# Kernel optimization log

Measured on AMD Instinct MI355X. Metric: run time of the kernel, lower is better.

The kernel has to match this reference:

```python
import jax, jax.numpy as jnp
import numpy as np

B, S, D, R, H = 4, 2048, 1024, 256, 8
NI, NP, NO, K = 8, 32, 8, 3
DH = R // H


def _householder_chain(x, vs):
    # x: [B,S,R], vs: [B,S,K,R]; apply K Householder reflections sequentially
    def step(carry, v):
        vn = v * jax.lax.rsqrt(jnp.sum(v * v, axis=-1, keepdims=True) + 1e-8)
        vTx = jnp.sum(carry * vn, axis=-1, keepdims=True)
        return carry - 2.0 * vn * vTx, None
    out, _ = jax.lax.scan(step, x, jnp.moveaxis(vs, 2, 0))
    return out


def _circuit_down(x, in_neurons, proc_neurons, input_weights, proc_idx):
    # soft mixture of input-neuron projections: d_model -> rank
    all_proj = jnp.einsum('bsd,ndr->bsnr', x, in_neurons)
    xr = jnp.einsum('bsnr,bsn->bsr', all_proj, input_weights)
    return _householder_chain(xr, proc_neurons[proc_idx])


def setup_inputs():
    key = jax.random.key(0)
    ks = jax.random.split(key, 14)
    n = lambda k, shape, sc: jax.random.normal(k, shape, jnp.float32) * sc
    inv_d, inv_r = 1.0 / np.sqrt(D), 1.0 / np.sqrt(R)
    return {
        'x': n(ks[0], (B, S, D), 1.0),
        'q_in': n(ks[1], (NI, D, R), inv_d),
        'q_proc': n(ks[2], (NP, R), inv_r),
        'k_in': n(ks[3], (NI, D, R), inv_d),
        'k_proc': n(ks[4], (NP, R), inv_r),
        'v_in': n(ks[5], (NI, D, R), inv_d),
        'v_proc': n(ks[6], (NP, R), inv_r),
        'o_proc': n(ks[7], (NP, R), inv_r),
        'o_out': n(ks[8], (NO, R, D), inv_r),
        'rd_in': n(ks[9], (NI, D), inv_d),
        'rd_proc': n(ks[10], (NP, D), inv_d),
        'ru_out': n(ks[11], (NO, R), inv_r),
        'ru_proc': n(ks[12], (NP, R), inv_r),
    }


def reference(x, q_in, q_proc, k_in, k_proc, v_in, v_proc, o_proc, o_out,
              rd_in, rd_proc, ru_out, ru_proc):
    # --- router (down): soft input weights + top-k process indices ---
    input_weights = jax.nn.softmax(x @ rd_in.T, axis=-1)          # [B,S,NI]
    _, pidx = jax.lax.top_k(x @ rd_proc.T, K)                     # [B,S,K]

    q = _circuit_down(x, q_in, q_proc, input_weights, pidx)      # [B,S,R]
    k = _circuit_down(x, k_in, k_proc, input_weights, pidx)
    v = _circuit_down(x, v_in, v_proc, input_weights, pidx)

    qh = q.reshape(B, S, H, DH)
    kh = k.reshape(B, S, H, DH)
    vh = v.reshape(B, S, H, DH)
    scores = jnp.einsum('bqhd,bkhd->bhqk', qh, kh) / np.sqrt(DH)
    attn = jax.nn.softmax(scores, axis=-1)
    o = jnp.einsum('bhqk,bkhd->bqhd', attn, vh).reshape(B, S, R)  # [B,S,R]

    # --- router (up): soft output weights + top-k process indices ---
    output_weights = jax.nn.softmax(o @ ru_out.T, axis=-1)        # [B,S,NO]
    _, pidx_u = jax.lax.top_k(o @ ru_proc.T, K)                   # [B,S,K]

    oh = _householder_chain(o, o_proc[pidx_u])                    # [B,S,R]
    out = jnp.einsum('bsr,bsn,nrd->bsd', oh, output_weights, o_out)
    return out
```

## Files before the change

kernel.cpp:

```cpp
#include <hip/hip_runtime.h>
#include <math.h>

#define NI 8
#define NP 32
#define TOPK 3

typedef _Float16 f16;
typedef f16 f16x8 __attribute__((ext_vector_type(8)));
typedef f16 f16x4 __attribute__((ext_vector_type(4)));
typedef float f32x4 __attribute__((ext_vector_type(4)));

__device__ __forceinline__ float wave_sum(float v) {
  #pragma unroll
  for (int off = 32; off; off >>= 1) v += __shfl_xor(v, off);
  return v;
}

__device__ __forceinline__ void gload16(const void* g, void* l) {
  __builtin_amdgcn_global_load_lds(
      (const __attribute__((address_space(1))) unsigned int*)g,
      (__attribute__((address_space(3))) unsigned int*)l, 16, 0, 0);
}

__device__ __forceinline__ void split4(float4 v, f16x4& h, f16x4& l) {
  h[0] = (f16)v.x; l[0] = (f16)(v.x - (float)h[0]);
  h[1] = (f16)v.y; l[1] = (f16)(v.y - (float)h[1]);
  h[2] = (f16)v.z; l[2] = (f16)(v.z - (float)h[2]);
  h[3] = (f16)v.w; l[3] = (f16)(v.w - (float)h[3]);
}

__device__ __forceinline__ unsigned int pack_f16x2(float x) {
  f16 h = (f16)x;
  f16 l = (f16)(x - (float)h);
  return (unsigned int)__builtin_bit_cast(unsigned short, h)
       | ((unsigned int)__builtin_bit_cast(unsigned short, l) << 16);
}

__device__ __forceinline__ void unpack8(const unsigned int* p, f16x8& hi, f16x8& lo) {
  uint4 w0 = *reinterpret_cast<const uint4*>(p);
  uint4 w1 = *reinterpret_cast<const uint4*>(p + 4);
  union { unsigned int u[4]; f16x8 v; } H, L;
  H.u[0] = (w0.x & 0xffffu) | (w0.y << 16);
  L.u[0] = (w0.x >> 16)     | (w0.y & 0xffff0000u);
  H.u[1] = (w0.z & 0xffffu) | (w0.w << 16);
  L.u[1] = (w0.z >> 16)     | (w0.w & 0xffff0000u);
  H.u[2] = (w1.x & 0xffffu) | (w1.y << 16);
  L.u[2] = (w1.x >> 16)     | (w1.y & 0xffff0000u);
  H.u[3] = (w1.z & 0xffffu) | (w1.w << 16);
  L.u[3] = (w1.z >> 16)     | (w1.w & 0xffff0000u);
  hi = H.v; lo = L.v;
}

template<int CHUNKS>
__global__ __launch_bounds__(256) void router_v2(
    const float* __restrict__ X,
    const float* __restrict__ Wsm,
    const float* __restrict__ Wtk,
    float* __restrict__ iw, int* __restrict__ pidx,
    f16* __restrict__ Xh, f16* __restrict__ Xl)
{
  const int Kin = CHUNKS * 256;
  const int tid = threadIdx.x, wave = tid >> 6, lane = tid & 63;
  __shared__ float sc[4][4][40];
  const size_t t0 = (size_t)blockIdx.x * 16 + wave * 4;

  float4 xv[4][CHUNKS];
  #pragma unroll
  for (int tt = 0; tt < 4; ++tt) {
    const float4* Xp = reinterpret_cast<const float4*>(X + (t0 + tt) * Kin);
    #pragma unroll
    for (int c = 0; c < CHUNKS; ++c) xv[tt][c] = Xp[c * 64 + lane];
  }
  if (Xh) {
    #pragma unroll
    for (int tt = 0; tt < 4; ++tt)
      #pragma unroll
      for (int c = 0; c < CHUNKS; ++c) {
        f16x4 h, l;
        split4(xv[tt][c], h, l);
        size_t off = (t0 + tt) * Kin + (c * 64 + lane) * 4;
        *reinterpret_cast<f16x4*>(Xh + off) = h;
        *reinterpret_cast<f16x4*>(Xl + off) = l;
      }
  }

  for (int w = 0; w < 40; ++w) {
    const float* Wr = (w < NI) ? (Wsm + (size_t)w * Kin) : (Wtk + (size_t)(w - NI) * Kin);
    const float4* Wp = reinterpret_cast<const float4*>(Wr);
    float p[4] = {};
    #pragma unroll
    for (int c = 0; c < CHUNKS; ++c) {
      float4 wv = Wp[c * 64 + lane];
      #pragma unroll
      for (int tt = 0; tt < 4; ++tt) {
        p[tt] = fmaf(xv[tt][c].x, wv.x, p[tt]);
        p[tt] = fmaf(xv[tt][c].y, wv.y, p[tt]);
        p[tt] = fmaf(xv[tt][c].z, wv.z, p[tt]);
        p[tt] = fmaf(xv[tt][c].w, wv.w, p[tt]);
      }
    }
    #pragma unroll
    for (int tt = 0; tt < 4; ++tt) {
      p[tt] = wave_sum(p[tt]);
      if (lane == 0) sc[wave][tt][w] = p[tt];
    }
  }

  for (int tt = 0; tt < 4; ++tt) {
    float s = (lane < NI) ? sc[wave][tt][lane] : -3.0e38f;
    float m = s;
    #pragma unroll
    for (int off = 4; off; off >>= 1) m = fmaxf(m, __shfl_xor(m, off));
    float e = expf(s - m);
    float sum = e;
    #pragma unroll
    for (int off = 4; off; off >>= 1) sum += __shfl_xor(sum, off);
    if (lane < NI) iw[(t0 + tt) * NI + lane] = e / sum;

    float v = (lane < NP) ? sc[wave][tt][NI + lane] : -3.0e38f;
    int idx = lane;
    #pragma unroll
    for (int j = 0; j < TOPK; ++j) {
      float bv = v; int bi = idx;
      #pragma unroll
      for (int off = 32; off; off >>= 1) {
        float ov = __shfl_xor(bv, off); int oi = __shfl_xor(bi, off);
        if (ov > bv || (ov == bv && oi < bi)) { bv = ov; bi = oi; }
      }
      if (lane == 0) pidx[(t0 + tt) * TOPK + j] = bi;
      if (idx == bi) v = -3.0e38f;
    }
  }
}

__global__ __launch_bounds__(256) void router_hh_up(
    const float* __restrict__ O,
    const float* __restrict__ Wsm,
    const float* __restrict__ Wtk,
    const float* __restrict__ Pm,
    float* __restrict__ owt, int* __restrict__ pidxu,
    f16* __restrict__ Oh, f16* __restrict__ Ol)
{
  const int tid = threadIdx.x, wave = tid >> 6, lane = tid & 63;
  __shared__ float sc[4][4][40];
  const size_t t0 = (size_t)blockIdx.x * 16 + wave * 4;

  float4 xv[4];
  #pragma unroll
  for (int tt = 0; tt < 4; ++tt)
    xv[tt] = *reinterpret_cast<const float4*>(O + (t0 + tt) * 256 + lane * 4);

  for (int w = 0; w < 40; ++w) {
    const float* Wr = (w < NI) ? (Wsm + (size_t)w * 256) : (Wtk + (size_t)(w - NI) * 256);
    float4 wv = *reinterpret_cast<const float4*>(Wr + lane * 4);
    float p[4];
    #pragma unroll
    for (int tt = 0; tt < 4; ++tt) {
      float q = 0.f;
      q = fmaf(xv[tt].x, wv.x, q); q = fmaf(xv[tt].y, wv.y, q);
      q = fmaf(xv[tt].z, wv.z, q); q = fmaf(xv[tt].w, wv.w, q);
      p[tt] = wave_sum(q);
    }
    #pragma unroll
    for (int tt = 0; tt < 4; ++tt)
      if (lane == 0) sc[wave][tt][w] = p[tt];
  }

  for (int tt = 0; tt < 4; ++tt) {
    float s = (lane < NI) ? sc[wave][tt][lane] : -3.0e38f;
    float m = s;
    #pragma unroll
    for (int off = 4; off; off >>= 1) m = fmaxf(m, __shfl_xor(m, off));
    float e = expf(s - m);
    float sum = e;
    #pragma unroll
    for (int off = 4; off; off >>= 1) sum += __shfl_xor(sum, off);
    if (lane < NI) owt[(t0 + tt) * NI + lane] = e / sum;

    float v = (lane < NP) ? sc[wave][tt][NI + lane] : -3.0e38f;
    int idx = lane;
    int pid[TOPK];
    #pragma unroll
    for (int j = 0; j < TOPK; ++j) {
      float bv = v; int bi = idx;
      #pragma unroll
      for (int off = 32; off; off >>= 1) {
        float ov = __shfl_xor(bv, off); int oi = __shfl_xor(bi, off);
        if (ov > bv || (ov == bv && oi < bi)) { bv = ov; bi = oi; }
      }
      pid[j] = bi;
      if (lane == 0) pidxu[(t0 + tt) * TOPK + j] = bi;
      if (idx == bi) v = -3.0e38f;
    }

    float4 x4 = xv[tt];
    #pragma unroll
    for (int j = 0; j < TOPK; ++j) {
      const float* vp = Pm + (size_t)pid[j] * 256;
      float4 v4 = *reinterpret_cast<const float4*>(vp + lane * 4);
      float ss = v4.x * v4.x + v4.y * v4.y + v4.z * v4.z + v4.w * v4.w;
      ss = wave_sum(ss);
      float inv = 1.0f / sqrtf(ss + 1e-8f);
      float4 vn = {v4.x * inv, v4.y * inv, v4.z * inv, v4.w * inv};
      float dt = vn.x * x4.x + vn.y * x4.y + vn.z * x4.z + vn.w * x4.w;
      dt = wave_sum(dt);
      float d2 = 2.0f * dt;
      x4.x = fmaf(-d2, vn.x, x4.x);
      x4.y = fmaf(-d2, vn.y, x4.y);
      x4.z = fmaf(-d2, vn.z, x4.z);
      x4.w = fmaf(-d2, vn.w, x4.w);
    }
    f16x4 h, l;
    split4(x4, h, l);
    *reinterpret_cast<f16x4*>(Oh + (t0 + tt) * 256 + lane * 4) = h;
    *reinterpret_cast<f16x4*>(Ol + (t0 + tt) * 256 + lane * 4) = l;
  }
}

__global__ __launch_bounds__(256) void pack_bt(
    const float* __restrict__ S, f16* __restrict__ Dh, f16* __restrict__ Dl,
    int C, int K)
{
  __shared__ float T[64][65];
  const int tid = threadIdx.x;
  const int kb = blockIdx.x * 64, cb = blockIdx.y * 64;
  const int tr = tid >> 4, tc = (tid & 15) * 4;
  #pragma unroll
  for (int i = 0; i < 4; ++i) {
    float4 v = *reinterpret_cast<const float4*>(&S[(size_t)(kb + tr + i * 16) * C + cb + tc]);
    T[tr + i * 16][tc + 0] = v.x; T[tr + i * 16][tc + 1] = v.y;
    T[tr + i * 16][tc + 2] = v.z; T[tr + i * 16][tc + 3] = v.w;
  }
  __syncthreads();
  #pragma unroll
  for (int i = 0; i < 4; ++i) {
    int c = tr + i * 16;
    f16x4 vh, vl;
    #pragma unroll
    for (int q = 0; q < 4; ++q) {
      float a = T[tc + q][c];
      f16 h = (f16)a;
      vh[q] = h;
      vl[q] = (f16)(a - (float)h);
    }
    *reinterpret_cast<f16x4*>(&Dh[(size_t)(cb + c) * K + kb + tc]) = vh;
    *reinterpret_cast<f16x4*>(&Dl[(size_t)(cb + c) * K + kb + tc]) = vl;
  }
}

#define TBM 128
#define TBK 32

template<int NFRAG>
__global__ __launch_bounds__(256, 3) void gemm_split2(
    const f16* __restrict__ Xh, const f16* __restrict__ Xl, int Kin,
    const float* __restrict__ W,
    const f16* __restrict__ Bth, const f16* __restrict__ Btl,
    float* __restrict__ C, int ldC, int Ktot)
{
  const int TBN = 32 * NFRAG;
  __shared__ f16x8 AhL[512];
  __shared__ f16x8 AlL[512];
  __shared__ f16x8 BhL[TBN * 4];
  __shared__ f16x8 BlL[TBN * 4];
  __shared__ float Ws[TBM][NI];

  const int tid = threadIdx.x;
  const int wave = tid >> 6, lane = tid & 63;
  const int wm = wave >> 1, wn = wave & 1;
  const int fr = lane & 15, ks = lane >> 4;
  const int row0 = blockIdx.x * TBM, c0 = blockIdx.y * TBN;

  for (int i = tid; i < TBM * NI; i += 256)
    Ws[i >> 3][i & 7] = W[(size_t)(row0 + (i >> 3)) * NI + (i & 7)];

  const int s1 = 256 + tid;
  const int ar0 = tid >> 2, kg0 = ((tid & 3) - (ar0 >> 1)) & 3;
  const int ar1 = s1 >> 2,  kg1 = ((s1 & 3) - (ar1 >> 1)) & 3;

  const f16* xh0 = Xh + (size_t)(row0 + ar0) * Kin + kg0 * 8;
  const f16* xh1 = Xh + (size_t)(row0 + ar1) * Kin + kg1 * 8;
  const f16* xl0 = Xl + (size_t)(row0 + ar0) * Kin + kg0 * 8;
  const f16* xl1 = Xl + (size_t)(row0 + ar1) * Kin + kg1 * 8;
  const f16* bh0 = Bth + (size_t)(c0 + ar0) * Ktot + kg0 * 8;
  const f16* bl0 = Btl + (size_t)(c0 + ar0) * Ktot + kg0 * 8;
  const int ar1b = (ar1 < TBN) ? ar1 : 0;
  const f16* bh1 = Bth + (size_t)(c0 + ar1b) * Ktot + kg1 * 8;
  const f16* bl1 = Btl + (size_t)(c0 + ar1b) * Ktot + kg1 * 8;
  const bool b2 = (NFRAG == 4) || (NFRAG == 3 && wave < 2);

  f16x8* AhW = &AhL[wave * 64];
  f16x8* AlW = &AlL[wave * 64];
  f16x8* BhW = &BhL[wave * 64];
  f16x8* BlW = &BlL[wave * 64];

  f32x4 acc[4][NFRAG] = {};
  f32x4 cac[4][NFRAG] = {};

  int n = 0, dk0 = 0;
  for (int kt = 0; kt < Ktot; kt += TBK) {
    __syncthreads();
    gload16(xh0 + dk0, AhW);
    gload16(xh1 + dk0, AhW + 256);
    gload16(xl0 + dk0, AlW);
    gload16(xl1 + dk0, AlW + 256);
    gload16(bh0 + kt, BhW);
    gload16(bl0 + kt, BlW);
    if (b2) {
      gload16(bh1 + kt, BhW + 256);
      gload16(bl1 + kt, BlW + 256);
    }
    __syncthreads();

    f16x8 ah[4], al[4], bh[NFRAG], bl[NFRAG];
    #pragma unroll
    for (int mf = 0; mf < 4; ++mf) {
      int ar = wm * 64 + mf * 16 + fr;
      int sl = ar * 4 + (((ar >> 1) + ks) & 3);
      ah[mf] = AhL[sl]; al[mf] = AlL[sl];
    }
    #pragma unroll
    for (int nf = 0; nf < NFRAG; ++nf) {
      int bc = wn * (16 * NFRAG) + nf * 16 + fr;
      int sl = bc * 4 + (((bc >> 1) + ks) & 3);
      bh[nf] = BhL[sl]; bl[nf] = BlL[sl];
    }
    #pragma unroll
    for (int mf = 0; mf < 4; ++mf)
      #pragma unroll
      for (int nf = 0; nf < NFRAG; ++nf) {
        acc[mf][nf] = __builtin_amdgcn_mfma_f32_16x16x32_f16(ah[mf], bh[nf], acc[mf][nf], 0, 0, 0);
        acc[mf][nf] = __builtin_amdgcn_mfma_f32_16x16x32_f16(ah[mf], bl[nf], acc[mf][nf], 0, 0, 0);
        acc[mf][nf] = __builtin_amdgcn_mfma_f32_16x16x32_f16(al[mf], bh[nf], acc[mf][nf], 0, 0, 0);
      }

    dk0 += TBK;
    if (dk0 == Kin) {
      dk0 = 0;
      #pragma unroll
      for (int mf = 0; mf < 4; ++mf) {
        float w0 = Ws[wm * 64 + mf * 16 + ks * 4 + 0][n];
        float w1 = Ws[wm * 64 + mf * 16 + ks * 4 + 1][n];
        float w2 = Ws[wm * 64 + mf * 16 + ks * 4 + 2][n];
        float w3 = Ws[wm * 64 + mf * 16 + ks * 4 + 3][n];
        #pragma unroll
        for (int nf = 0; nf < NFRAG; ++nf) {
          cac[mf][nf][0] = fmaf(w0, acc[mf][nf][0], cac[mf][nf][0]);
          cac[mf][nf][1] = fmaf(w1, acc[mf][nf][1], cac[mf][nf][1]);
          cac[mf][nf][2] = fmaf(w2, acc[mf][nf][2], cac[mf][nf][2]);
          cac[mf][nf][3] = fmaf(w3, acc[mf][nf][3], cac[mf][nf][3]);
          acc[mf][nf] = (f32x4){0.f, 0.f, 0.f, 0.f};
        }
      }
      ++n;
    }
  }

  #pragma unroll
  for (int mf = 0; mf < 4; ++mf)
    #pragma unroll
    for (int nf = 0; nf < NFRAG; ++nf) {
      int col = c0 + wn * (16 * NFRAG) + nf * 16 + fr;
      #pragma unroll
      for (int j = 0; j < 4; ++j) {
        int row = row0 + wm * 64 + mf * 16 + ks * 4 + j;
        C[(size_t)row * ldC + col] = cac[mf][nf][j];
      }
    }
}

#define GBM 128
#define GBN 128
#define GBK 16
#define GBMp 132

__global__ __launch_bounds__(256) void gemm_mix(
    const float* __restrict__ X, int Kin,
    const float* __restrict__ W,
    const float* __restrict__ Bm0, const float* __restrict__ Bm1, const float* __restrict__ Bm2,
    int ldB, float* __restrict__ C, int ldC, int Nz)
{
  __shared__ float As[GBK][GBMp];
  __shared__ float Bs[GBK][GBMp];
  __shared__ float Ws[GBM][NI];
  const int tid = threadIdx.x;
  const int row0 = blockIdx.x * GBM;
  const int z = blockIdx.z;
  const float* Bm = (z == 0) ? Bm0 : (z == 1) ? Bm1 : Bm2;
  const int c0 = blockIdx.y * GBN;
  for (int i = tid; i < GBM * NI; i += 256)
    Ws[i >> 3][i & 7] = W[(size_t)(row0 + (i >> 3)) * NI + (i & 7)];
  __syncthreads();

  float acc[8][8] = {};
  const int tr = tid >> 4, tc = tid & 15;
  const int srow = tid >> 2;
  const int sseg = (tid & 3) * 4;
  const int bk = tid >> 4;
  const int bc = (tid & 15) * 4;

  const int Ktot = Kin * NI;
  int n = 0, dk0 = 0;
  for (int kt = 0; kt < Ktot; kt += GBK) {
    __syncthreads();
    #pragma unroll
    for (int p = 0; p < 2; ++p) {
      int r = p * 64 + srow;
      float4 xv = *reinterpret_cast<const float4*>(&X[(size_t)(row0 + r) * Kin + dk0 + sseg]);
      float wgt = Ws[r][n];
      As[sseg + 0][r] = xv.x * wgt;
      As[sseg + 1][r] = xv.y * wgt;
      As[sseg + 2][r] = xv.z * wgt;
      As[sseg + 3][r] = xv.w * wgt;
    }
    #pragma unroll
    for (int p = 0; p < 2; ++p) {
      int cc = p * 64 + bc;
      float4 bv = *reinterpret_cast<const float4*>(&Bm[(size_t)(kt + bk) * ldB + c0 + cc]);
      *reinterpret_cast<float4*>(&Bs[bk][cc]) = bv;
    }
    __syncthreads();
    #pragma unroll
    for (int k = 0; k < GBK; ++k) {
      float4 a0 = *reinterpret_cast<const float4*>(&As[k][tr * 8]);
      float4 a1 = *reinterpret_cast<const float4*>(&As[k][tr * 8 + 4]);
      float4 b0 = *reinterpret_cast<const float4*>(&Bs[k][tc * 8]);
      float4 b1 = *reinterpret_cast<const float4*>(&Bs[k][tc * 8 + 4]);
      float av[8] = {a0.x, a0.y, a0.z, a0.w, a1.x, a1.y, a1.z, a1.w};
      float bv[8] = {b0.x, b0.y, b0.z, b0.w, b1.x, b1.y, b1.z, b1.w};
      #pragma unroll
      for (int i = 0; i < 8; ++i)
        #pragma unroll
        for (int j = 0; j < 8; ++j)
          acc[i][j] = fmaf(av[i], bv[j], acc[i][j]);
    }
    dk0 += GBK;
    if (dk0 == Kin) { dk0 = 0; ++n; }
  }
  #pragma unroll
  for (int i = 0; i < 8; ++i) {
    int row = row0 + tr * 8 + i;
    float* Cp = C + (size_t)row * ldC + z * Nz + c0 + tc * 8;
    float4 o0 = {acc[i][0], acc[i][1], acc[i][2], acc[i][3]};
    float4 o1 = {acc[i][4], acc[i][5], acc[i][6], acc[i][7]};
    *reinterpret_cast<float4*>(Cp) = o0;
    *reinterpret_cast<float4*>(Cp + 4) = o1;
  }
}

__global__ __launch_bounds__(256) void hh_kernel(
    float* __restrict__ X, int ldX,
    const float* __restrict__ P0, const float* __restrict__ P1, const float* __restrict__ P2,
    const int* __restrict__ pidx,
    unsigned int* __restrict__ Vpk)
{
  const int tid = threadIdx.x, wave = tid >> 6, lane = tid & 63;
  const int t = blockIdx.x * 4 + wave;
  const int circ = blockIdx.y;
  const float* P = (circ == 0) ? P0 : (circ == 1) ? P1 : P2;
  float* xp = X + (size_t)t * ldX + circ * 256;
  float4 x4 = *reinterpret_cast<float4*>(xp + lane * 4);
  #pragma unroll
  for (int j = 0; j < TOPK; ++j) {
    int id = pidx[t * TOPK + j];
    const float* vp = P + (size_t)id * 256;
    float4 v4 = *reinterpret_cast<const float4*>(vp + lane * 4);
    float ss = v4.x * v4.x + v4.y * v4.y + v4.z * v4.z + v4.w * v4.w;
    ss = wave_sum(ss);
    float inv = 1.0f / sqrtf(ss + 1e-8f);
    float4 vn = {v4.x * inv, v4.y * inv, v4.z * inv, v4.w * inv};
    float dt = vn.x * x4.x + vn.y * x4.y + vn.z * x4.z + vn.w * x4.w;
    dt = wave_sum(dt);
    float d2 = 2.0f * dt;
    x4.x = fmaf(-d2, vn.x, x4.x);
    x4.y = fmaf(-d2, vn.y, x4.y);
    x4.z = fmaf(-d2, vn.z, x4.z);
    x4.w = fmaf(-d2, vn.w, x4.w);
  }
  if (circ == 2 && Vpk) {
    uint4 pk = {pack_f16x2(x4.x), pack_f16x2(x4.y), pack_f16x2(x4.z), pack_f16x2(x4.w)};
    *reinterpret_cast<uint4*>(Vpk + (size_t)t * 256 + lane * 4) = pk;
  } else {
    *reinterpret_cast<float4*>(xp + lane * 4) = x4;
  }
}

__global__ __launch_bounds__(256, 2) void attn_mfma(
    const float* __restrict__ qkv, const unsigned int* __restrict__ Vpk,
    float* __restrict__ O)
{
  __shared__ f16 Kh[64][40];
  __shared__ f16 Kl[64][40];
  __shared__ unsigned int Vtp[32][68];
  __shared__ unsigned int Pp[4][32][68];

  const int tid = threadIdx.x, wave = tid >> 6, lane = tid & 63;
  const int c = lane & 15, g = lane >> 4;
  const int bh = blockIdx.y, b = bh >> 3, h = bh & 7;
  const int q0 = blockIdx.x * 128;
  const size_t tbase = (size_t)b * 2048;
  const float SCALE = 0.17677669529663687f;

  f16x8 qh[2], ql[2];
  #pragma unroll
  for (int qt = 0; qt < 2; ++qt) {
    const int row = q0 + wave * 32 + qt * 16 + c;
    const float* qp = qkv + (tbase + row) * 768 + h * 32 + g * 8;
    float4 a = *reinterpret_cast<const float4*>(qp);
    float4 b4 = *reinterpret_cast<const float4*>(qp + 4);
    float qv[8] = {a.x, a.y, a.z, a.w, b4.x, b4.y, b4.z, b4.w};
    #pragma unroll
    for (int j = 0; j < 8; ++j) {
      float xs = qv[j] * SCALE;
      f16 hh = (f16)xs;
      qh[qt][j] = hh;
      ql[qt][j] = (f16)(xs - (float)hh);
    }
  }

  const int kj = tid >> 2, dq = (tid & 3) * 8;
  const int vk = tid & 63, vq = (tid >> 6) * 8;

  float4 rka, rkb;
  uint4 rv0, rv1;
  {
    const float* kp = qkv + (tbase + kj) * 768 + 256 + h * 32 + dq;
    rka = *reinterpret_cast<const float4*>(kp);
    rkb = *reinterpret_cast<const float4*>(kp + 4);
    const unsigned int* vp = Vpk + (tbase + vk) * 256 + h * 32 + vq;
    rv0 = *reinterpret_cast<const uint4*>(vp);
    rv1 = *reinterpret_cast<const uint4*>(vp + 4);
  }

  f32x4 sacc[2][4];
  f32x4 oacc[2][2] = {};
  float mrow[2][4] = {{-INFINITY, -INFINITY, -INFINITY, -INFINITY},
                      {-INFINITY, -INFINITY, -INFINITY, -INFINITY}};
  float lrow[2][4] = {};

  for (int k0 = 0; k0 < 2048; k0 += 64) {
    __syncthreads();
    {
      float kv[8] = {rka.x, rka.y, rka.z, rka.w, rkb.x, rkb.y, rkb.z, rkb.w};
      f16x8 khi, klo;
      #pragma unroll
      for (int j = 0; j < 8; ++j) {
        f16 hh = (f16)kv[j];
        khi[j] = hh;
        klo[j] = (f16)(kv[j] - (float)hh);
      }
      *reinterpret_cast<f16x8*>(&Kh[kj][dq]) = khi;
      *reinterpret_cast<f16x8*>(&Kl[kj][dq]) = klo;

      Vtp[vq + 0][vk] = rv0.x; Vtp[vq + 1][vk] = rv0.y;
      Vtp[vq + 2][vk] = rv0.z; Vtp[vq + 3][vk] = rv0.w;
      Vtp[vq + 4][vk] = rv1.x; Vtp[vq + 5][vk] = rv1.y;
      Vtp[vq + 6][vk] = rv1.z; Vtp[vq + 7][vk] = rv1.w;
    }
    __syncthreads();
    if (k0 + 64 < 2048) {
      const float* kp = qkv + (tbase + k0 + 64 + kj) * 768 + 256 + h * 32 + dq;
      rka = *reinterpret_cast<const float4*>(kp);
      rkb = *reinterpret_cast<const float4*>(kp + 4);
      const unsigned int* vp = Vpk + (tbase + k0 + 64 + vk) * 256 + h * 32 + vq;
      rv0 = *reinterpret_cast<const uint4*>(vp);
      rv1 = *reinterpret_cast<const uint4*>(vp + 4);
    }

    #pragma unroll
    for (int s = 0; s < 4; ++s) {
      f16x8 kbh = *reinterpret_cast<const f16x8*>(&Kh[s * 16 + c][g * 8]);
      f16x8 kbl = *reinterpret_cast<const f16x8*>(&Kl[s * 16 + c][g * 8]);
      #pragma unroll
      for (int qt = 0; qt < 2; ++qt) {
        f32x4 acc = {0.f, 0.f, 0.f, 0.f};
        acc = __builtin_amdgcn_mfma_f32_16x16x32_f16(qh[qt], kbh, acc, 0, 0, 0);
        acc = __builtin_amdgcn_mfma_f32_16x16x32_f16(qh[qt], kbl, acc, 0, 0, 0);
        acc = __builtin_amdgcn_mfma_f32_16x16x32_f16(ql[qt], kbh, acc, 0, 0, 0);
        sacc[qt][s] = acc;
      }
    }

    float alpha[2][4];
    #pragma unroll
    for (int qt = 0; qt < 2; ++qt)
      #pragma unroll
      for (int r = 0; r < 4; ++r) {
        float mt = fmaxf(fmaxf(sacc[qt][0][r], sacc[qt][1][r]),
                         fmaxf(sacc[qt][2][r], sacc[qt][3][r]));
        #pragma unroll
        for (int off = 1; off < 16; off <<= 1) mt = fmaxf(mt, __shfl_xor(mt, off));
        float mn = fmaxf(mrow[qt][r], mt);
        float al = __expf(mrow[qt][r] - mn);
        mrow[qt][r] = mn;
        alpha[qt][r] = al;
        float ps = 0.f;
        #pragma unroll
        for (int s = 0; s < 4; ++s) {
          float p = __expf(sacc[qt][s][r] - mn);
          sacc[qt][s][r] = p;
          ps += p;
        }
        #pragma unroll
        for (int off = 1; off < 16; off <<= 1) ps += __shfl_xor(ps, off);
        lrow[qt][r] = lrow[qt][r] * al + ps;
      }

    #pragma unroll
    for (int qt = 0; qt < 2; ++qt)
      #pragma unroll
      for (int s = 0; s < 4; ++s)
        #pragma unroll
        for (int r = 0; r < 4; ++r)
          Pp[wave][qt * 16 + g * 4 + r][s * 16 + c] = pack_f16x2(sacc[qt][s][r]);

    #pragma unroll
    for (int qt = 0; qt < 2; ++qt)
      #pragma unroll
      for (int dh = 0; dh < 2; ++dh)
        #pragma unroll
        for (int r = 0; r < 4; ++r) oacc[qt][dh][r] *= alpha[qt][r];

    #pragma unroll
    for (int ch = 0; ch < 2; ++ch) {
      f16x8 pah[2], pal[2];
      #pragma unroll
      for (int qt = 0; qt < 2; ++qt)
        unpack8(&Pp[wave][qt * 16 + c][ch * 32 + g * 8], pah[qt], pal[qt]);
      #pragma unroll
      for (int dh = 0; dh < 2; ++dh) {
        f16x8 vh, vl;
        unpack8(&Vtp[dh * 16 + c][ch * 32 + g * 8], vh, vl);
        #pragma unroll
        for (int qt = 0; qt < 2; ++qt) {
          oacc[qt][dh] = __builtin_amdgcn_mfma_f32_16x16x32_f16(pah[qt], vh, oacc[qt][dh], 0, 0, 0);
          oacc[qt][dh] = __builtin_amdgcn_mfma_f32_16x16x32_f16(pah[qt], vl, oacc[qt][dh], 0, 0, 0);
          oacc[qt][dh] = __builtin_amdgcn_mfma_f32_16x16x32_f16(pal[qt], vh, oacc[qt][dh], 0, 0, 0);
        }
      }
    }
  }

  #pragma unroll
  for (int qt = 0; qt < 2; ++qt)
    #pragma unroll
    for (int r = 0; r < 4; ++r) {
      float inv = 1.0f / lrow[qt][r];
      int row = q0 + wave * 32 + qt * 16 + g * 4 + r;
      #pragma unroll
      for (int dh = 0; dh < 2; ++dh)
        O[(tbase + row) * 256 + h * 32 + dh * 16 + c] = oacc[qt][dh][r] * inv;
    }
}

__global__ __launch_bounds__(256) void attn_kernel(
    const float* __restrict__ qkv, float* __restrict__ O)
{
  const int tid = threadIdx.x;
  const int wave = tid >> 6, lane = tid & 63;
  const int bh = blockIdx.y, b = bh >> 3, h = bh & 7;
  const int q0 = blockIdx.x * 8;
  const size_t tbase = (size_t)b * 2048;
  const float SCALE = 0.17677669529663687f;

  __shared__ float Ks[64][36];
  __shared__ float Vt[32][68];
  __shared__ float Ps[4][2][64];

  const int wq = __builtin_amdgcn_readfirstlane(wave);
  const float* qr0 = qkv + (tbase + q0 + wq * 2) * 768 + h * 32;
  float qa[32], qb[32];
  #pragma unroll
  for (int i = 0; i < 32; ++i) { qa[i] = qr0[i]; qb[i] = qr0[768 + i]; }

  const int r = lane >> 5, d = lane & 31;
  float m0 = -INFINITY, m1 = -INFINITY, l0 = 0.f, l1 = 0.f, oacc = 0.f;

  for (int k0 = 0; k0 < 2048; k0 += 64) {
    __syncthreads();
    {
      int j = tid >> 2;
      int c = (tid & 3) * 8;
      const float* kp = qkv + (tbase + k0 + j) * 768 + 256 + h * 32 + c;
      float4 ka = *reinterpret_cast<const float4*>(kp);
      float4 kb = *reinterpret_cast<const float4*>(kp + 4);
      *reinterpret_cast<float4*>(&Ks[j][c]) = ka;
      *reinterpret_cast<float4*>(&Ks[j][c + 4]) = kb;
      const float* vp = qkv + (tbase + k0 + j) * 768 + 512 + h * 32 + c;
      float4 va = *reinterpret_cast<const float4*>(vp);
      float4 vb = *reinterpret_cast<const float4*>(vp + 4);
      Vt[c + 0][j] = va.x; Vt[c + 1][j] = va.y; Vt[c + 2][j] = va.z; Vt[c + 3][j] = va.w;
      Vt[c + 4][j] = vb.x; Vt[c + 5][j] = vb.y; Vt[c + 6][j] = vb.z; Vt[c + 7][j] = vb.w;
    }
    __syncthreads();
    float s0 = 0.f, s1 = 0.f;
    #pragma unroll
    for (int dd = 0; dd < 8; ++dd) {
      float4 kv = *reinterpret_cast<const float4*>(&Ks[lane][dd * 4]);
      s0 = fmaf(qa[dd * 4 + 0], kv.x, s0); s1 = fmaf(qb[dd * 4 + 0], kv.x, s1);
      s0 = fmaf(qa[dd * 4 + 1], kv.y, s0); s1 = fmaf(qb[dd * 4 + 1], kv.y, s1);
      s0 = fmaf(qa[dd * 4 + 2], kv.z, s0); s1 = fmaf(qb[dd * 4 + 2], kv.z, s1);
      s0 = fmaf(qa[dd * 4 + 3], kv.w, s0); s1 = fmaf(qb[dd * 4 + 3], kv.w, s1);
    }
    s0 *= SCALE; s1 *= SCALE;
    float mx0 = s0, mx1 = s1;
    #pragma unroll
    for (int off = 32; off; off >>= 1) {
      mx0 = fmaxf(mx0, __shfl_xor(mx0, off));
      mx1 = fmaxf(mx1, __shfl_xor(mx1, off));
    }
    float nm0 = fmaxf(m0, mx0), nm1 = fmaxf(m1, mx1);
    float p0 = expf(s0 - nm0), p1 = expf(s1 - nm1);
    float a0 = expf(m0 - nm0), a1 = expf(m1 - nm1);
    float sp0 = p0, sp1 = p1;
    #pragma unroll
    for (int off = 32; off; off >>= 1) {
      sp0 += __shfl_xor(sp0, off);
      sp1 += __shfl_xor(sp1, off);
    }
    l0 = l0 * a0 + sp0; l1 = l1 * a1 + sp1;
    m0 = nm0; m1 = nm1;
    Ps[wave][0][lane] = p0; Ps[wave][1][lane] = p1;
    oacc *= (r == 0) ? a0 : a1;
    #pragma unroll
    for (int jq = 0; jq < 16; ++jq) {
      float4 pv = *reinterpret_cast<const float4*>(&Ps[wave][r][jq * 4]);
      float4 vv = *reinterpret_cast<const float4*>(&Vt[d][jq * 4]);
      oacc = fmaf(pv.x, vv.x, oacc);
      oacc = fmaf(pv.y, vv.y, oacc);
      oacc = fmaf(pv.z, vv.z, oacc);
      oacc = fmaf(pv.w, vv.w, oacc);
    }
  }
  float lf = (r == 0) ? l0 : l1;
  oacc /= lf;
  O[(tbase + q0 + wave * 2 + r) * 256 + h * 32 + d] = oacc;
}

extern "C" void kernel_launch(void* const* d_in, const int* in_sizes, int n_in,
                              void* d_out, int out_size, void* d_ws, size_t ws_size,
                              hipStream_t stream) {
  const float* x       = (const float*)d_in[0];
  const float* q_in    = (const float*)d_in[1];
  const float* q_proc  = (const float*)d_in[2];
  const float* k_in    = (const float*)d_in[3];
  const float* k_proc  = (const float*)d_in[4];
  const float* v_in    = (const float*)d_in[5];
  const float* v_proc  = (const float*)d_in[6];
  const float* o_proc  = (const float*)d_in[7];
  const float* o_out   = (const float*)d_in[8];
  const float* rd_in   = (const float*)d_in[9];
  const float* rd_proc = (const float*)d_in[10];
  const float* ru_out  = (const float*)d_in[11];
  const float* ru_proc = (const float*)d_in[12];
  float* out = (float*)d_out;
  float* qkv = (float*)d_out;

  const size_t NEED2 = (768ull << 10) + 768ull * 8192 * 2 * 2 + 8192ull * 1024 * 2 * 2;

  if (ws_size >= NEED2) {
    char* wsb = (char*)d_ws;
    float* iw    = (float*)wsb;
    float* owt   = (float*)(wsb + (256 << 10));
    int*   pidx  = (int*)(wsb + (512 << 10));
    int*   pidxu = (int*)(wsb + (640 << 10));
    char*  R1    = wsb + (768 << 10);
    f16* bth_q = (f16*)R1;
    f16* btl_q = (f16*)(R1 + 768ull * 8192 * 2);
    char*  R2    = R1 + 768ull * 8192 * 2 * 2;
    f16* Xh = (f16*)R2;
    f16* Xl = (f16*)(R2 + 8192ull * 1024 * 2);
    float* obuf  = (float*)R2;
    f16* Oh    = (f16*)(R2 + 8388608);
    f16* Ol    = (f16*)(R2 + 12582912);
    f16* bth_o = (f16*)(R2 + 16777216);
    f16* btl_o = (f16*)(R2 + 20971520);
    unsigned int* Vpk = (unsigned int*)((char*)d_out + 25165824);

    router_v2<4><<<dim3(512), dim3(256), 0, stream>>>(x, rd_in, rd_proc, iw, pidx, Xh, Xl);
    pack_bt<<<dim3(128, 4), dim3(256), 0, stream>>>(q_in, bth_q,                 btl_q,                 256, 8192);
    pack_bt<<<dim3(128, 4), dim3(256), 0, stream>>>(k_in, bth_q + 256ull * 8192, btl_q + 256ull * 8192, 256, 8192);
    pack_bt<<<dim3(128, 4), dim3(256), 0, stream>>>(v_in, bth_q + 512ull * 8192, btl_q + 512ull * 8192, 256, 8192);
    gemm_split2<3><<<dim3(64, 8), dim3(256), 0, stream>>>(Xh, Xl, 1024, iw, bth_q, btl_q,
                                                          qkv, 768, 8192);
    hh_kernel<<<dim3(2048, 3), dim3(256), 0, stream>>>(qkv, 768, q_proc, k_proc, v_proc, pidx,
                                                       Vpk);
    pack_bt<<<dim3(32, 16), dim3(256), 0, stream>>>(o_out, bth_o, btl_o, 1024, 2048);
    attn_mfma<<<dim3(16, 32), dim3(256), 0, stream>>>(qkv, Vpk, obuf);
    router_hh_up<<<dim3(512), dim3(256), 0, stream>>>(obuf, ru_out, ru_proc, o_proc,
                                                      owt, pidxu, Oh, Ol);
    gemm_split2<4><<<dim3(64, 8), dim3(256), 0, stream>>>(Oh, Ol, 256, owt, bth_o, btl_o,
                                                          out, 1024, 2048);
  } else {
    float* ws = (float*)d_ws;
    float* iw    = ws;
    int*   pidx  = (int*)(ws + 65536);
    float* obuf  = ws + 65536 + 24576;
    float* owt   = obuf + 8192 * 256;
    int*   pidxu = (int*)(owt + 65536);

    router_v2<4><<<dim3(512), dim3(256), 0, stream>>>(x, rd_in, rd_proc, iw, pidx,
                                                      (f16*)nullptr, (f16*)nullptr);
    gemm_mix<<<dim3(64, 2, 3), dim3(256), 0, stream>>>(x, 1024, iw, q_in, k_in, v_in,
                                                       256, qkv, 768, 256);
    hh_kernel<<<dim3(2048, 3), dim3(256), 0, stream>>>(qkv, 768, q_proc, k_proc, v_proc, pidx,
                                                       (unsigned int*)nullptr);
    attn_kernel<<<dim3(256, 32), dim3(256), 0, stream>>>(qkv, obuf);
    router_v2<1><<<dim3(512), dim3(256), 0, stream>>>(obuf, ru_out, ru_proc, owt, pidxu,
                                                      (f16*)nullptr, (f16*)nullptr);
    hh_kernel<<<dim3(2048, 1), dim3(256), 0, stream>>>(obuf, 256, o_proc, o_proc, o_proc, pidxu,
                                                       (unsigned int*)nullptr);
    gemm_mix<<<dim3(64, 8, 1), dim3(256), 0, stream>>>(obuf, 256, owt, o_out, o_out, o_out,
                                                       1024, out, 1024, 1024);
  }
}
```

Baseline: 729.4 us.

## Add K=64 tiled split-fp16 GEMM for QKV and shrink output GEMM tile

Adds a new gemm_k64 kernel for the QKV down-projection. Each step loads a 64-deep K slice into swizzled LDS, and the 128x64 output tiles run on a 64x12 grid instead of 64x8. The output-projection GEMM changes from NFRAG=4 to NFRAG=2 with twice as many blocks. The aim is fewer K-loop iterations and barriers per tile and more blocks to fill the CUs, at the cost of more LDS per block and more reloads of the A operand across column tiles.

```diff
diff --git a/kernel.cpp b/kernel.cpp
--- a/kernel.cpp
+++ b/kernel.cpp
@@ -246,6 +246,124 @@
     *reinterpret_cast<f16x4*>(&Dh[(size_t)(cb + c) * K + kb + tc]) = vh;
     *reinterpret_cast<f16x4*>(&Dl[(size_t)(cb + c) * K + kb + tc]) = vl;
   }
+}
+
+__global__ __launch_bounds__(256, 3) void gemm_k64(
+    const f16* __restrict__ Xh, const f16* __restrict__ Xl, int Kin,
+    const float* __restrict__ W,
+    const f16* __restrict__ Bth, const f16* __restrict__ Btl,
+    float* __restrict__ C, int ldC, int Ktot)
+{
+  __shared__ f16x8 AhL[1024];
+  __shared__ f16x8 AlL[1024];
+  __shared__ f16x8 BhL[512];
+  __shared__ f16x8 BlL[512];
+  __shared__ float Ws[128][NI];
+
+  const int tid = threadIdx.x;
+  const int wave = tid >> 6, lane = tid & 63;
+  const int wm = wave >> 1, wn = wave & 1;
+  const int fr = lane & 15, ks = lane >> 4;
+  const int row0 = blockIdx.x * 128, c0 = blockIdx.y * 64;
+
+  for (int i = tid; i < 128 * NI; i += 256)
+    Ws[i >> 3][i & 7] = W[(size_t)(row0 + (i >> 3)) * NI + (i & 7)];
+
+  const f16* xhp[4];
+  const f16* xlp[4];
+  #pragma unroll
+  for (int i = 0; i < 4; ++i) {
+    int s = i * 256 + tid;
+    int r = s >> 3, kg = ((s & 7) - (r >> 1)) & 7;
+    xhp[i] = Xh + (size_t)(row0 + r) * Kin + kg * 8;
+    xlp[i] = Xl + (size_t)(row0 + r) * Kin + kg * 8;
+  }
+  const f16* bhp[2];
+  const f16* blp[2];
+  #pragma unroll
+  for (int i = 0; i < 2; ++i) {
+    int s = i * 256 + tid;
+    int cc = s >> 3, kg = ((s & 7) - (cc >> 1)) & 7;
+    bhp[i] = Bth + (size_t)(c0 + cc) * Ktot + kg * 8;
+    blp[i] = Btl + (size_t)(c0 + cc) * Ktot + kg * 8;
+  }
+
+  f32x4 acc[4][2] = {};
+  f32x4 cac[4][2] = {};
+
+  int n = 0, dk0 = 0;
+  for (int kt = 0; kt < Ktot; kt += 64) {
+    __syncthreads();
+    #pragma unroll
+    for (int i = 0; i < 4; ++i) {
+      gload16(xhp[i] + dk0, &AhL[i * 256 + wave * 64]);
+      gload16(xlp[i] + dk0, &AlL[i * 256 + wave * 64]);
+    }
+    #pragma unroll
+    for (int i = 0; i < 2; ++i) {
+      gload16(bhp[i] + kt, &BhL[i * 256 + wave * 64]);
+      gload16(blp[i] + kt, &BlL[i * 256 + wave * 64]);
+    }
+    __syncthreads();
+
+    #pragma unroll
+    for (int kk = 0; kk < 2; ++kk) {
+      f16x8 ah[4], al[4], bh[2], bl[2];
+      #pragma unroll
+      for (int mf = 0; mf < 4; ++mf) {
+        int ar = wm * 64 + mf * 16 + fr;
+        int sl = ar * 8 + (((ar >> 1) + kk * 4 + ks) & 7);
+        ah[mf] = AhL[sl]; al[mf] = AlL[sl];
+      }
+      #pragma unroll
+      for (int nf = 0; nf < 2; ++nf) {
+        int bc = wn * 32 + nf * 16 + fr;
+        int sl = bc * 8 + (((bc >> 1) + kk * 4 + ks) & 7);
+        bh[nf] = BhL[sl]; bl[nf] = BlL[sl];
+      }
+      #pragma unroll
+      for (int mf = 0; mf < 4; ++mf)
+        #pragma unroll
+        for (int nf = 0; nf < 2; ++nf) {
+          acc[mf][nf] = __builtin_amdgcn_mfma_f32_16x16x32_f16(ah[mf], bh[nf], acc[mf][nf], 0, 0, 0);
+          acc[mf][nf] = __builtin_amdgcn_mfma_f32_16x16x32_f16(ah[mf], bl[nf], acc[mf][nf], 0, 0, 0);
+          acc[mf][nf] = __builtin_amdgcn_mfma_f32_16x16x32_f16(al[mf], bh[nf], acc[mf][nf], 0, 0, 0);
+        }
+    }
+
+    dk0 += 64;
+    if (dk0 == Kin) {
+      dk0 = 0;
+      #pragma unroll
+      for (int mf = 0; mf < 4; ++mf) {
+        float w0 = Ws[wm * 64 + mf * 16 + ks * 4 + 0][n];
+        float w1 = Ws[wm * 64 + mf * 16 + ks * 4 + 1][n];
+        float w2 = Ws[wm * 64 + mf * 16 + ks * 4 + 2][n];
+        float w3 = Ws[wm * 64 + mf * 16 + ks * 4 + 3][n];
+        #pragma unroll
+        for (int nf = 0; nf < 2; ++nf) {
+          cac[mf][nf][0] = fmaf(w0, acc[mf][nf][0], cac[mf][nf][0]);
+          cac[mf][nf][1] = fmaf(w1, acc[mf][nf][1], cac[mf][nf][1]);
+          cac[mf][nf][2] = fmaf(w2, acc[mf][nf][2], cac[mf][nf][2]);
+          cac[mf][nf][3] = fmaf(w3, acc[mf][nf][3], cac[mf][nf][3]);
+          acc[mf][nf] = (f32x4){0.f, 0.f, 0.f, 0.f};
+        }
+      }
+      ++n;
+    }
+  }
+
+  #pragma unroll
+  for (int mf = 0; mf < 4; ++mf)
+    #pragma unroll
+    for (int nf = 0; nf < 2; ++nf) {
+      int col = c0 + wn * 32 + nf * 16 + fr;
+      #pragma unroll
+      for (int j = 0; j < 4; ++j) {
+        int row = row0 + wm * 64 + mf * 16 + ks * 4 + j;
+        C[(size_t)row * ldC + col] = cac[mf][nf][j];
+      }
+    }
 }
 
 #define TBM 128
@@ -781,16 +899,16 @@
     pack_bt<<<dim3(128, 4), dim3(256), 0, stream>>>(q_in, bth_q,                 btl_q,                 256, 8192);
     pack_bt<<<dim3(128, 4), dim3(256), 0, stream>>>(k_in, bth_q + 256ull * 8192, btl_q + 256ull * 8192, 256, 8192);
     pack_bt<<<dim3(128, 4), dim3(256), 0, stream>>>(v_in, bth_q + 512ull * 8192, btl_q + 512ull * 8192, 256, 8192);
-    gemm_split2<3><<<dim3(64, 8), dim3(256), 0, stream>>>(Xh, Xl, 1024, iw, bth_q, btl_q,
-                                                          qkv, 768, 8192);
+    gemm_k64<<<dim3(64, 12), dim3(256), 0, stream>>>(Xh, Xl, 1024, iw, bth_q, btl_q,
+                                                     qkv, 768, 8192);
     hh_kernel<<<dim3(2048, 3), dim3(256), 0, stream>>>(qkv, 768, q_proc, k_proc, v_proc, pidx,
                                                        Vpk);
     pack_bt<<<dim3(32, 16), dim3(256), 0, stream>>>(o_out, bth_o, btl_o, 1024, 2048);
     attn_mfma<<<dim3(16, 32), dim3(256), 0, stream>>>(qkv, Vpk, obuf);
     router_hh_up<<<dim3(512), dim3(256), 0, stream>>>(obuf, ru_out, ru_proc, o_proc,
                                                       owt, pidxu, Oh, Ol);
-    gemm_split2<4><<<dim3(64, 8), dim3(256), 0, stream>>>(Oh, Ol, 256, owt, bth_o, btl_o,
-                                                          out, 1024, 2048);
+    gemm_split2<2><<<dim3(64, 16), dim3(256), 0, stream>>>(Oh, Ol, 256, owt, bth_o, btl_o,
+                                                           out, 1024, 2048);
   } else {
     float* ws = (float*)d_ws;
     float* iw    = ws;
```

Result: faster. 701.5 us (median of 2 runs) (-3.8%).
